# Optimization experiments

Measured on AMD Instinct MI355X. Metric: run time of the kernel, lower is better.

The kernel has to match this reference:

```python
import jax, jax.numpy as jnp
import numpy as np

NUM_HEADS = 12
LN_EPS = 1e-5
SM_EPS = 1e-6


def layer_norm(x, w, b):
    m = x.mean(-1, keepdims=True)
    v = ((x - m) ** 2).mean(-1, keepdims=True)
    return (x - m) / jnp.sqrt(v + LN_EPS) * w + b


def softmax_with_policy(attn, policy):
    # attn: [B,H,N,N], policy: [B,N,1]
    B, H, N, _ = attn.shape
    attn_policy = policy.reshape(B, 1, 1, N)
    eye = jnp.eye(N, dtype=attn.dtype)[None, None]
    attn_policy = attn_policy + (1.0 - attn_policy) * eye
    m = attn.max(axis=-1, keepdims=True)
    e = jnp.exp(attn - m) * attn_policy
    return (e + SM_EPS / N) / (e.sum(axis=-1, keepdims=True) + SM_EPS)


def create_ys(ncdf, n_ref):
    # ncdf: [B, N-1]; returns ys: [B, n_ref-1]
    B = ncdf.shape[0]
    ys = jnp.linspace(0.0, 1.0, n_ref - 1, dtype=ncdf.dtype)[None, :]
    ys_start = jnp.min(ncdf + (ncdf == 0).astype(ncdf.dtype) * 1e8, axis=1, keepdims=True)
    steps = jnp.arange(n_ref - 1, dtype=ncdf.dtype)[None, :]
    return ys_start + (ys * (n_ref - 2) - ys_start * steps) / (n_ref - 2)


def get_unique_indices(indices, max_value):
    # duplicate indices are replaced by max_value, then re-sorted
    B = indices.shape[0]
    s = jnp.sort(indices, axis=1)
    shifted = jnp.concatenate([s[:, 1:], jnp.ones((B, 1), s.dtype)], axis=1)
    uniq = jnp.where(shifted == s, max_value, s)
    return jnp.sort(uniq, axis=1)


def ats_block(x, policy, norm1_w, norm1_b, qkv_w, proj_w, proj_b,
              norm2_w, norm2_b, fc1_w, fc1_b, fc2_w, fc2_b,
              n_tokens, n_ref_tokens):
    B, N, C = x.shape
    H = NUM_HEADS
    dh = C // H
    scale = dh ** -0.5

    xn = layer_norm(x, norm1_w, norm1_b)
    qkv = (xn @ qkv_w).reshape(B, N, 3, H, dh).transpose(2, 0, 3, 1, 4)  # [3,B,H,N,dh]
    qkv = qkv * policy[None, :, None, :, :]
    q, k, v = qkv[0], qkv[1], qkv[2]

    attn = softmax_with_policy(jnp.einsum('bhnd,bhmd->bhnm', q, k) * scale, policy)

    # --- score assignment ---
    v_norm = jnp.linalg.norm(v.transpose(0, 2, 1, 3).reshape(B, N, C), axis=2)  # [B,N]
    sig = attn[:, :, 0, :].sum(axis=1) * v_norm      # CLS attention row summed over heads
    sig = sig[:, 1:]
    sig = sig / sig.sum(axis=1, keepdims=True)
    order = jnp.argsort(sig, axis=1)                 # ascending
    sorted_scores = jnp.take_along_axis(sig, order, axis=1)

    # --- inverse transform sampling ---
    cdf = jnp.cumsum(sorted_scores, axis=1)
    cmin = cdf.min(axis=1, keepdims=True)
    cmax = cdf.max(axis=1, keepdims=True)
    ncdf = (cdf - cmin) / (cmax - cmin)              # [B, N-1]
    ys = create_ys(ncdf, n_ref_tokens)               # [B, n_ref-1]
    diff = (n_ref_tokens - 1) - (N - 1)
    ncdf_p = jnp.pad(ncdf, ((0, 0), (diff, 0))) if diff > 0 else ncdf
    tokens_to_pick = jnp.argmin(jnp.abs(ys[:, :, None] - ncdf_p[:, None, :]), axis=2) - diff

    uniq = get_unique_indices(tokens_to_pick, N - 1)[:, :N - 1]
    ui = uniq[:, :n_tokens - 1]                      # [B, n_tokens-1]

    # reorder attn rows / raw tokens by significance order, pad a zero row at N-1
    oidx = jnp.broadcast_to(order[:, None, :, None], (B, H, N - 1, N))
    attn_sorted = jnp.take_along_axis(attn[:, :, 1:, :], oidx, axis=2)
    attn_tmp = jnp.pad(attn_sorted, ((0, 0), (0, 0), (0, 1), (0, 0)))
    rx_sorted = jnp.take_along_axis(x[:, 1:, :], jnp.broadcast_to(order[:, :, None], (B, N - 1, C)), axis=1)
    rx_tmp = jnp.pad(rx_sorted, ((0, 0), (0, 1), (0, 0)))

    uidx = jnp.broadcast_to(ui[:, None, :, None], (B, H, n_tokens - 1, N))
    attn_sel = jnp.take_along_axis(attn_tmp, uidx, axis=2)
    rx_sel = jnp.take_along_axis(rx_tmp, jnp.broadcast_to(ui[:, :, None], (B, n_tokens - 1, C)), axis=1)

    attn_new = jnp.concatenate([attn[:, :, 0:1, :], attn_sel], axis=2)     # [B,H,n_tokens,N]
    selected_x = jnp.concatenate([x[:, 0:1, :], rx_sel], axis=1)           # [B,n_tokens,C]
    pol_new = (ui != N - 1).astype(x.dtype)[:, :, None]
    pol_new = jnp.pad(pol_new, ((0, 0), (1, 0), (0, 0)), constant_values=1.0)  # [B,n_tokens,1]

    out = jnp.einsum('bhnm,bhmd->bhnd', attn_new, v)
    out = out.transpose(0, 2, 1, 3).reshape(B, n_tokens, C)
    out = (out @ proj_w + proj_b) * pol_new

    x2 = selected_x + out
    h = jax.nn.gelu(layer_norm(x2, norm2_w, norm2_b) @ fc1_w + fc1_b, approximate=False)
    x2 = x2 + (h @ fc2_w + fc2_b) * pol_new
    return x2, pol_new


def setup_inputs() -> dict:
    key = jax.random.key(0)
    ks = jax.random.split(key, 6)
    B, N, C = 8, 785, 768
    init = lambda k, sh, fan: jax.random.normal(k, sh, jnp.float32) * (fan ** -0.5)
    return {
        'x': jax.random.normal(ks[0], (B, N, C), jnp.float32),
        'policy': jnp.ones((B, N, 1), jnp.float32),
        'norm1_w': jnp.ones((C,), jnp.float32),
        'norm1_b': jnp.zeros((C,), jnp.float32),
        'qkv_w': init(ks[1], (C, 3 * C), C),
        'proj_w': init(ks[2], (C, C), C),
        'proj_b': jnp.zeros((C,), jnp.float32),
        'norm2_w': jnp.ones((C,), jnp.float32),
        'norm2_b': jnp.zeros((C,), jnp.float32),
        'fc1_w': init(ks[3], (C, 4 * C), C),
        'fc1_b': jnp.zeros((4 * C,), jnp.float32),
        'fc2_w': init(ks[4], (4 * C, C), 4 * C),
        'fc2_b': jnp.zeros((C,), jnp.float32),
        'n_tokens': 393,
        'n_ref_tokens': 785,
    }


def reference(x, policy, norm1_w, norm1_b, qkv_w, proj_w, proj_b,
              norm2_w, norm2_b, fc1_w, fc1_b, fc2_w, fc2_b,
              n_tokens, n_ref_tokens):
    return ats_block(x, policy, norm1_w, norm1_b, qkv_w, proj_w, proj_b,
                     norm2_w, norm2_b, fc1_w, fc1_b, fc2_w, fc2_b,
                     int(n_tokens), int(n_ref_tokens))
```

## Files before the change

kernel.cpp:

```cpp
#include <hip/hip_runtime.h>
#include <hip/hip_bf16.h>
#include <float.h>
#include <math.h>
#include <stdint.h>

constexpr int B_   = 8;
constexpr int N_   = 785;
constexpr int C_   = 768;
constexpr int H_   = 12;
constexpr int DH_  = 64;
constexpr int NT_  = 393;
constexpr int QKVC = 3 * C_;
constexpr int BN   = B_ * N_;
constexpr int BT   = B_ * NT_;
constexpr int MSEL = N_ - 1;
constexpr float  SCALE_F = 0.125f;
constexpr double LNEPS   = 1e-5;
constexpr double SMEPS   = 1e-6;

#define DEV static __device__ __forceinline__

typedef __hip_bfloat16 bf16;
typedef __attribute__((ext_vector_type(8))) short frag8;
typedef __attribute__((ext_vector_type(4))) float facc4;

DEV double blockReduceSumD(double v, double* scratch, int nw) {
#pragma unroll
  for (int o = 32; o; o >>= 1) v += __shfl_xor(v, o);
  int lane = threadIdx.x & 63, wid = threadIdx.x >> 6;
  __syncthreads();
  if (lane == 0) scratch[wid] = v;
  __syncthreads();
  double r = scratch[0];
  for (int i = 1; i < nw; i++) r += scratch[i];
  return r;
}
DEV double blockReduceMaxD(double v, double* scratch, int nw) {
#pragma unroll
  for (int o = 32; o; o >>= 1) v = fmax(v, __shfl_xor(v, o));
  int lane = threadIdx.x & 63, wid = threadIdx.x >> 6;
  __syncthreads();
  if (lane == 0) scratch[wid] = v;
  __syncthreads();
  double r = scratch[0];
  for (int i = 1; i < nw; i++) r = fmax(r, scratch[i]);
  return r;
}
DEV float blockReduceSumF(float v, float* scratch, int nw) {
#pragma unroll
  for (int o = 32; o; o >>= 1) v += __shfl_xor(v, o);
  int lane = threadIdx.x & 63, wid = threadIdx.x >> 6;
  __syncthreads();
  if (lane == 0) scratch[wid] = v;
  __syncthreads();
  float r = scratch[0];
  for (int i = 1; i < nw; i++) r += scratch[i];
  return r;
}
DEV float blockReduceMaxF(float v, float* scratch, int nw) {
#pragma unroll
  for (int o = 32; o; o >>= 1) v = fmaxf(v, __shfl_xor(v, o));
  int lane = threadIdx.x & 63, wid = threadIdx.x >> 6;
  __syncthreads();
  if (lane == 0) scratch[wid] = v;
  __syncthreads();
  float r = scratch[0];
  for (int i = 1; i < nw; i++) r = fmaxf(r, scratch[i]);
  return r;
}

__global__ __launch_bounds__(256) void ln1_kernel(
    const float* __restrict__ x, const float* __restrict__ w, const float* __restrict__ b,
    double* __restrict__ xn64, bf16* __restrict__ xnb) {
  int row = blockIdx.x;
  int t = threadIdx.x;
  __shared__ double scr[8];
  const float* xr = x + (size_t)row * C_;
  double vals[3];
#pragma unroll
  for (int i = 0; i < 3; i++) vals[i] = (double)xr[t + i * 256];
  double s = vals[0] + vals[1] + vals[2];
  s = blockReduceSumD(s, scr, 4);
  double mean = s / (double)C_;
  double vs = 0.0;
#pragma unroll
  for (int i = 0; i < 3; i++) { double d = vals[i] - mean; vs += d * d; }
  vs = blockReduceSumD(vs, scr, 4);
  double inv = 1.0 / sqrt(vs / (double)C_ + LNEPS);
#pragma unroll
  for (int i = 0; i < 3; i++) {
    int c = t + i * 256;
    double o = (vals[i] - mean) * inv * (double)w[c] + (double)b[c];
    xn64[(size_t)row * C_ + c] = o;
    xnb[(size_t)row * C_ + c] = __float2bfloat16((float)o);
  }
}

__global__ __launch_bounds__(256) void transpose_bf16(
    const float* __restrict__ W, bf16* __restrict__ Wt, int K, int N) {
  __shared__ float tile[32][33];
  int k0 = blockIdx.y * 32, n0 = blockIdx.x * 32;
  int tx = threadIdx.x & 31, ty = threadIdx.x >> 5;
  for (int i = ty; i < 32; i += 8) {
    int k = k0 + i, n = n0 + tx;
    tile[i][tx] = (k < K && n < N) ? W[(size_t)k * N + n] : 0.f;
  }
  __syncthreads();
  for (int i = ty; i < 32; i += 8) {
    int n = n0 + i, k = k0 + tx;
    if (n < N && k < K) Wt[(size_t)n * K + k] = __float2bfloat16(tile[tx][i]);
  }
}

__global__ __launch_bounds__(256) void gemm_bf16(
    const bf16* __restrict__ A, const bf16* __restrict__ Bt,
    float* __restrict__ Cc, const float* __restrict__ bias,
    const float* __restrict__ rowscale, int M, int K, int Ncols) {
  __shared__ short As[64][40];
  __shared__ short Bs[64][40];
  const short* Ap = (const short*)A;
  const short* Bp = (const short*)Bt;
  int t = threadIdx.x;
  int n0 = blockIdx.x * 64;
  int m0 = blockIdx.y * 64;
  int w = t >> 6, l = t & 63;
  int srow = t >> 2;
  int koff = (t & 3) * 8;
  facc4 acc[4] = {{0, 0, 0, 0}, {0, 0, 0, 0}, {0, 0, 0, 0}, {0, 0, 0, 0}};
  int frow = (l & 15);
  int fk = (l >> 4) * 8;
  for (int k0 = 0; k0 < K; k0 += 32) {
    {
      int4 av = make_int4(0, 0, 0, 0);
      if (m0 + srow < M)
        av = *(const int4*)(Ap + (size_t)(m0 + srow) * K + k0 + koff);
      *(int4*)(&As[srow][koff]) = av;
      int4 bv = *(const int4*)(Bp + (size_t)(n0 + srow) * K + k0 + koff);
      *(int4*)(&Bs[srow][koff]) = bv;
    }
    __syncthreads();
    frag8 a = *(frag8*)(&As[w * 16 + frow][fk]);
#pragma unroll
    for (int nt = 0; nt < 4; nt++) {
      frag8 bfr = *(frag8*)(&Bs[nt * 16 + frow][fk]);
      acc[nt] = __builtin_amdgcn_mfma_f32_16x16x32_bf16(a, bfr, acc[nt], 0, 0, 0);
    }
    __syncthreads();
  }
#pragma unroll
  for (int nt = 0; nt < 4; nt++) {
#pragma unroll
    for (int reg = 0; reg < 4; reg++) {
      int row = m0 + w * 16 + (l >> 4) * 4 + reg;
      int col = n0 + nt * 16 + (l & 15);
      if (row < M) {
        float v = acc[nt][reg];
        if (bias) v += bias[col];
        if (rowscale) v *= rowscale[row];
        Cc[(size_t)row * Ncols + col] = v;
      }
    }
  }
}

__global__ __launch_bounds__(256) void q0_kernel(
    const double* __restrict__ xn64, const float* __restrict__ qkvw,
    const float* __restrict__ policy, double* __restrict__ q064) {
  int b = blockIdx.x;
  int jc = blockIdx.y;
  int t = threadIdx.x;
  int jl = t & 63, ks = t >> 6;
  __shared__ double x0[C_];
  __shared__ double part[4][64];
  for (int i = t; i < C_; i += 256) x0[i] = xn64[(size_t)(b * N_) * C_ + i];
  __syncthreads();
  int j = jc * 64 + jl;
  const float* wp = qkvw + j;
  double a = 0.0;
  int c0 = ks * 192;
#pragma unroll 8
  for (int c = c0; c < c0 + 192; c++) a += x0[c] * (double)wp[(size_t)c * QKVC];
  part[ks][jl] = a;
  __syncthreads();
  if (t < 64) {
    double pol = (double)policy[b * N_];
    q064[b * C_ + jc * 64 + t] =
        (part[0][t] + part[1][t] + part[2][t] + part[3][t]) * pol;
  }
}

__global__ __launch_bounds__(256) void g_kernel(
    const double* __restrict__ q064, const float* __restrict__ qkvw,
    double* __restrict__ g64) {
  int bh = blockIdx.x;
  int b = bh / H_, h = bh % H_;
  int t = threadIdx.x;
  __shared__ double qh[DH_];
  if (t < DH_) qh[t] = q064[b * C_ + h * DH_ + t];
  __syncthreads();
  for (int c = t; c < C_; c += 256) {
    const float* wp = qkvw + (size_t)c * QKVC + C_ + h * DH_;
    double a = 0.0;
#pragma unroll 8
    for (int d = 0; d < DH_; d++) a += qh[d] * (double)wp[d];
    g64[(size_t)bh * C_ + c] = a;
  }
}

__global__ __launch_bounds__(256) void logits_kernel(
    const double* __restrict__ xn64, const double* __restrict__ g64,
    const float* __restrict__ policy, double* __restrict__ l64) {
  int row = blockIdx.x;
  int b = row / N_;
  int n = row % N_;
  int t = threadIdx.x;
  int w = t >> 6, lane = t & 63;
  __shared__ double xr[C_];
  for (int i = t; i < C_; i += 256) xr[i] = xn64[(size_t)row * C_ + i];
  __syncthreads();
  double pol = (double)policy[row];
#pragma unroll
  for (int hh = 0; hh < 3; hh++) {
    int h = w + hh * 4;
    const double* gp = g64 + (size_t)(b * H_ + h) * C_;
    double p = 0.0;
#pragma unroll 4
    for (int i = lane; i < C_; i += 64) p += xr[i] * gp[i];
#pragma unroll
    for (int o = 32; o; o >>= 1) p += __shfl_xor(p, o);
    if (lane == 0) l64[(size_t)(b * H_ + h) * N_ + n] = 0.125 * pol * p;
  }
}

__global__ __launch_bounds__(256) void vnorm_kernel(
    const double* __restrict__ xn64, const float* __restrict__ qkvw,
    double* __restrict__ vnp3) {
  __shared__ double scr[8];
  int r0 = blockIdx.x * 8;
  int chunk = blockIdx.y;
  int t = threadIdx.x;
  double acc[8] = {};
  const double* xb = xn64 + (size_t)r0 * C_;
  const float* wcol = qkvw + 2 * C_ + chunk * 256 + t;
  for (int c = 0; c < C_; c += 2) {
    double w0 = (double)wcol[(size_t)c * QKVC];
    double w1 = (double)wcol[(size_t)(c + 1) * QKVC];
#pragma unroll
    for (int r = 0; r < 8; r++) {
      double x0 = xb[(size_t)r * C_ + c];
      double x1 = xb[(size_t)r * C_ + c + 1];
      acc[r] += x0 * w0;
      acc[r] += x1 * w1;
    }
  }
#pragma unroll
  for (int r = 0; r < 8; r++) {
    double p = acc[r] * acc[r];
    double s = blockReduceSumD(p, scr, 4);
    if (t == 0) vnp3[(size_t)chunk * BN + r0 + r] = s;
  }
}

__global__ __launch_bounds__(256) void vnorm_combine_kernel(
    const double* __restrict__ vnp3, const float* __restrict__ policy,
    double* __restrict__ vnorm2) {
  int row = blockIdx.x * 256 + threadIdx.x;
  if (row >= BN) return;
  double s = vnp3[row] + vnp3[(size_t)BN + row] + vnp3[(size_t)2 * BN + row];
  double pol = (double)policy[row];
  vnorm2[row] = s * pol * pol;
}

__global__ __launch_bounds__(256) void softmax0_kernel(
    double* __restrict__ l64, const float* __restrict__ policy) {
  int bh = blockIdx.x;
  int b = bh / H_;
  double* lp = l64 + (size_t)bh * N_;
  __shared__ double scr[8];
  int t = threadIdx.x;
  double mx = -1e300;
  for (int n = t; n < N_; n += 256) mx = fmax(mx, lp[n]);
  mx = blockReduceMaxD(mx, scr, 4);
  double ssum = 0.0;
  for (int n = t; n < N_; n += 256) {
    double pol = (double)policy[b * N_ + n];
    double w = (n == 0) ? 1.0 : pol;
    double e = exp(lp[n] - mx) * w;
    lp[n] = e;
    ssum += e;
  }
  ssum = blockReduceSumD(ssum, scr, 4);
  double denom = ssum + SMEPS;
  double addc = SMEPS / (double)N_;
  for (int n = t; n < N_; n += 256) lp[n] = (lp[n] + addc) / denom;
}

__global__ __launch_bounds__(1024) void select_kernel(
    const double* __restrict__ p0, const double* __restrict__ vnorm2,
    int* __restrict__ selidx, float* __restrict__ poln, float* __restrict__ out_pol) {
  int b = blockIdx.x;
  int t = threadIdx.x;
  __shared__ double sigv[MSEL];
  __shared__ double svals[MSEL];
  __shared__ double nc[MSEL];
  __shared__ int    ord[MSEL];
  __shared__ int    pick[MSEL];
  __shared__ int    spick[MSEL];
  __shared__ int    uq[MSEL];
  __shared__ int    suq[MSEL];
  __shared__ double sh_ys;

  if (t < MSEL) {
    int n = t + 1;
    double s = 0.0;
#pragma unroll
    for (int h = 0; h < H_; h++) s += p0[(size_t)(b * H_ + h) * N_ + n];
    sigv[t] = s * sqrt(vnorm2[b * N_ + n]);
  }
  __syncthreads();
  if (t < MSEL) {
    double v = sigv[t];
    int rank = 0;
    for (int i = 0; i < MSEL; i++) {
      double vi = sigv[i];
      rank += (vi < v) || (vi == v && i < t);
    }
    ord[rank] = t;
    svals[rank] = v;
  }
  __syncthreads();
  if (t == 0) {
    double a = 0.0;
    for (int i = 0; i < MSEL; i++) { a += svals[i]; svals[i] = a; }
  }
  __syncthreads();
  {
    double c0 = svals[0], cN = svals[MSEL - 1];
    if (t < MSEL) nc[t] = (svals[t] - c0) / (cN - c0);
  }
  __syncthreads();
  if (t == 0) {
    double m = 1e300;
    for (int i = 0; i < MSEL; i++) {
      double v = nc[i];
      if (v == 0.0) v += 100000000.0;
      m = fmin(m, v);
    }
    sh_ys = m;
  }
  __syncthreads();
  if (t < MSEL) {
    double s = sh_ys;
    double ysj = (t == MSEL - 1) ? 1.0 : (double)t / 783.0;
    double y = s + (ysj * 783.0 - s * (double)t) / 783.0;
    double bd = 1e300;
    int bi = 0;
    for (int i = 0; i < MSEL; i++) {
      double d = fabs(y - nc[i]);
      if (d < bd) { bd = d; bi = i; }
    }
    pick[t] = bi;
  }
  __syncthreads();
  if (t < MSEL) {
    int p = pick[t];
    int rank = 0;
    for (int i = 0; i < MSEL; i++) {
      int pi = pick[i];
      rank += (pi < p) || (pi == p && i < t);
    }
    spick[rank] = p;
  }
  __syncthreads();
  if (t < MSEL) {
    int s = spick[t];
    int nxt = (t < MSEL - 1) ? spick[t + 1] : 1;
    uq[t] = (nxt == s) ? MSEL : s;
  }
  __syncthreads();
  if (t < MSEL) {
    int u = uq[t];
    int rank = 0;
    for (int i = 0; i < MSEL; i++) {
      int ui = uq[i];
      rank += (ui < u) || (ui == u && i < t);
    }
    suq[rank] = u;
  }
  __syncthreads();
  if (t < NT_) {
    int sel, polI;
    if (t == 0) { sel = 0; polI = 1; }
    else {
      int ut = suq[t - 1];
      polI = (ut != MSEL) ? 1 : 0;
      sel = polI ? (ord[ut] + 1) : -1;
    }
    selidx[b * NT_ + t] = sel;
    poln[b * NT_ + t] = (float)polI;
    out_pol[b * NT_ + t] = (float)polI;
  }
}

__global__ __launch_bounds__(256) void flash_kernel(
    const float* __restrict__ qkv, const int* __restrict__ selidx,
    const float* __restrict__ policy, bf16* __restrict__ attn_bf) {
  int bh = blockIdx.y;
  int b = bh / H_, h = bh % H_;
  int j0 = blockIdx.x * 64;
  int t = threadIdx.x;
  __shared__ float Qs[64][68];
  __shared__ float KVs[64][68];
  __shared__ float Ps[64][68];
  __shared__ float Vsum[64];
  int lm = t >> 2;
  int kb = (t & 3) * 16;
  {
    int j = j0 + lm;
    int r = (j < NT_) ? selidx[b * NT_ + j] : -1;
    if (r < 0) r = 0;
    const float* qp = qkv + (size_t)(b * N_ + r) * QKVC + h * DH_ + kb;
    float4 v0 = *(const float4*)(qp + 0);
    float4 v1 = *(const float4*)(qp + 4);
    float4 v2 = *(const float4*)(qp + 8);
    float4 v3 = *(const float4*)(qp + 12);
    Qs[kb + 0][lm] = v0.x; Qs[kb + 1][lm] = v0.y; Qs[kb + 2][lm] = v0.z; Qs[kb + 3][lm] = v0.w;
    Qs[kb + 4][lm] = v1.x; Qs[kb + 5][lm] = v1.y; Qs[kb + 6][lm] = v1.z; Qs[kb + 7][lm] = v1.w;
    Qs[kb + 8][lm] = v2.x; Qs[kb + 9][lm] = v2.y; Qs[kb +10][lm] = v2.z; Qs[kb +11][lm] = v2.w;
    Qs[kb +12][lm] = v3.x; Qs[kb +13][lm] = v3.y; Qs[kb +14][lm] = v3.z; Qs[kb +15][lm] = v3.w;
  }
  if (t < 64) Vsum[t] = 0.f;
  int tm = (t >> 4) << 2, tn = (t & 15) << 2;
  int rrow[4];
#pragma unroll
  for (int i = 0; i < 4; i++) {
    int j = j0 + tm + i;
    rrow[i] = (j < NT_) ? selidx[b * NT_ + j] : -1;
  }
  float m_run[4] = {-1e30f, -1e30f, -1e30f, -1e30f};
  float s_run[4] = {0.f, 0.f, 0.f, 0.f};
  float O[4][4] = {{0.f}};
  for (int n0 = 0; n0 < 832; n0 += 64) {
    __syncthreads();
    {
      int n = n0 + lm;
      bool ok = n < N_;
      const float* kp = qkv + (size_t)(b * N_ + (ok ? n : 0)) * QKVC + C_ + h * DH_ + kb;
      float4 v0 = ok ? *(const float4*)(kp + 0)  : make_float4(0, 0, 0, 0);
      float4 v1 = ok ? *(const float4*)(kp + 4)  : make_float4(0, 0, 0, 0);
      float4 v2 = ok ? *(const float4*)(kp + 8)  : make_float4(0, 0, 0, 0);
      float4 v3 = ok ? *(const float4*)(kp + 12) : make_float4(0, 0, 0, 0);
      KVs[kb + 0][lm] = v0.x; KVs[kb + 1][lm] = v0.y; KVs[kb + 2][lm] = v0.z; KVs[kb + 3][lm] = v0.w;
      KVs[kb + 4][lm] = v1.x; KVs[kb + 5][lm] = v1.y; KVs[kb + 6][lm] = v1.z; KVs[kb + 7][lm] = v1.w;
      KVs[kb + 8][lm] = v2.x; KVs[kb + 9][lm] = v2.y; KVs[kb +10][lm] = v2.z; KVs[kb +11][lm] = v2.w;
      KVs[kb +12][lm] = v3.x; KVs[kb +13][lm] = v3.y; KVs[kb +14][lm] = v3.z; KVs[kb +15][lm] = v3.w;
    }
    __syncthreads();
    float S[4][4] = {{0.f}};
#pragma unroll 16
    for (int k = 0; k < 64; k++) {
      float a0 = Qs[k][tm + 0], a1 = Qs[k][tm + 1], a2 = Qs[k][tm + 2], a3 = Qs[k][tm + 3];
      float b0 = KVs[k][tn + 0], b1 = KVs[k][tn + 1], b2 = KVs[k][tn + 2], b3 = KVs[k][tn + 3];
      S[0][0] += a0 * b0; S[0][1] += a0 * b1; S[0][2] += a0 * b2; S[0][3] += a0 * b3;
      S[1][0] += a1 * b0; S[1][1] += a1 * b1; S[1][2] += a1 * b2; S[1][3] += a1 * b3;
      S[2][0] += a2 * b0; S[2][1] += a2 * b1; S[2][2] += a2 * b2; S[2][3] += a2 * b3;
      S[3][0] += a3 * b0; S[3][1] += a3 * b1; S[3][2] += a3 * b2; S[3][3] += a3 * b3;
    }
    float tmax[4];
#pragma unroll
    for (int i = 0; i < 4; i++) {
      float mx = -1e30f;
#pragma unroll
      for (int jj = 0; jj < 4; jj++) {
        int n = n0 + tn + jj;
        float v = (n < N_) ? S[i][jj] * SCALE_F : -1e30f;
        S[i][jj] = v;
        mx = fmaxf(mx, v);
      }
      tmax[i] = mx;
    }
#pragma unroll
    for (int o = 1; o < 16; o <<= 1) {
#pragma unroll
      for (int i = 0; i < 4; i++) tmax[i] = fmaxf(tmax[i], __shfl_xor(tmax[i], o));
    }
    float m_new[4], scl[4], psum[4];
#pragma unroll
    for (int i = 0; i < 4; i++) {
      m_new[i] = fmaxf(m_run[i], tmax[i]);
      scl[i] = expf(m_run[i] - m_new[i]);
      psum[i] = 0.f;
    }
    float polv[4];
#pragma unroll
    for (int jj = 0; jj < 4; jj++) {
      int n = n0 + tn + jj;
      polv[jj] = (n < N_) ? policy[b * N_ + n] : 0.f;
    }
#pragma unroll
    for (int i = 0; i < 4; i++) {
#pragma unroll
      for (int jj = 0; jj < 4; jj++) {
        int n = n0 + tn + jj;
        float w = (n == rrow[i]) ? 1.f : polv[jj];
        float e = expf(S[i][jj] - m_new[i]) * w;
        S[i][jj] = e;
        psum[i] += e;
      }
    }
#pragma unroll
    for (int o = 1; o < 16; o <<= 1) {
#pragma unroll
      for (int i = 0; i < 4; i++) psum[i] += __shfl_xor(psum[i], o);
    }
#pragma unroll
    for (int i = 0; i < 4; i++) {
      s_run[i] = s_run[i] * scl[i] + psum[i];
      m_run[i] = m_new[i];
    }
    __syncthreads();
#pragma unroll
    for (int i = 0; i < 4; i++) {
#pragma unroll
      for (int jj = 0; jj < 4; jj++) Ps[tn + jj][tm + i] = S[i][jj];
    }
    {
      int n = n0 + lm;
      bool ok = n < N_;
      const float* vp = qkv + (size_t)(b * N_ + (ok ? n : 0)) * QKVC + 2 * C_ + h * DH_ + kb;
      float4 v0 = ok ? *(const float4*)(vp + 0)  : make_float4(0, 0, 0, 0);
      float4 v1 = ok ? *(const float4*)(vp + 4)  : make_float4(0, 0, 0, 0);
      float4 v2 = ok ? *(const float4*)(vp + 8)  : make_float4(0, 0, 0, 0);
      float4 v3 = ok ? *(const float4*)(vp + 12) : make_float4(0, 0, 0, 0);
      *(float4*)(&KVs[lm][kb + 0])  = v0;
      *(float4*)(&KVs[lm][kb + 4])  = v1;
      *(float4*)(&KVs[lm][kb + 8])  = v2;
      *(float4*)(&KVs[lm][kb + 12]) = v3;
    }
    __syncthreads();
    if (t < 64) {
      float a = 0.f;
#pragma unroll 16
      for (int k = 0; k < 64; k++) a += KVs[k][t];
      Vsum[t] += a;
    }
#pragma unroll
    for (int i = 0; i < 4; i++) {
#pragma unroll
      for (int jj = 0; jj < 4; jj++) O[i][jj] *= scl[i];
    }
#pragma unroll 16
    for (int k = 0; k < 64; k++) {
      float a0 = Ps[k][tm + 0], a1 = Ps[k][tm + 1], a2 = Ps[k][tm + 2], a3 = Ps[k][tm + 3];
      float b0 = KVs[k][tn + 0], b1 = KVs[k][tn + 1], b2 = KVs[k][tn + 2], b3 = KVs[k][tn + 3];
      O[0][0] += a0 * b0; O[0][1] += a0 * b1; O[0][2] += a0 * b2; O[0][3] += a0 * b3;
      O[1][0] += a1 * b0; O[1][1] += a1 * b1; O[1][2] += a1 * b2; O[1][3] += a1 * b3;
      O[2][0] += a2 * b0; O[2][1] += a2 * b1; O[2][2] += a2 * b2; O[2][3] += a2 * b3;
      O[3][0] += a3 * b0; O[3][1] += a3 * b1; O[3][2] += a3 * b2; O[3][3] += a3 * b3;
    }
  }
  __syncthreads();
  float addc = 1e-6f / (float)N_;
#pragma unroll
  for (int i = 0; i < 4; i++) {
    int j = j0 + tm + i;
    if (j >= NT_) continue;
    float denom = s_run[i] + 1e-6f;
#pragma unroll
    for (int jj = 0; jj < 4; jj++) {
      float val = (O[i][jj] + addc * Vsum[tn + jj]) / denom;
      attn_bf[(size_t)(b * NT_ + j) * C_ + h * DH_ + tn + jj] = __float2bfloat16(val);
    }
  }
}

__global__ __launch_bounds__(256) void e2_kernel(
    const float* __restrict__ cbuf, const float* __restrict__ poln,
    const int* __restrict__ selidx, const float* __restrict__ x, float* __restrict__ x2) {
  int row = blockIdx.x;
  int t = threadIdx.x;
  int b = row / NT_;
  int r = selidx[row];
  float pn = poln[row];
  for (int i = t; i < C_; i += 256) {
    float sx = (r >= 0) ? x[(size_t)(b * N_ + r) * C_ + i] : 0.f;
    x2[(size_t)row * C_ + i] = sx + cbuf[(size_t)row * C_ + i] * pn;
  }
}

__global__ __launch_bounds__(256) void ln2_kernel(
    const float* __restrict__ xin, const float* __restrict__ w, const float* __restrict__ b,
    bf16* __restrict__ xoutb) {
  int row = blockIdx.x;
  int t = threadIdx.x;
  __shared__ float scr[8];
  const float* xr = xin + (size_t)row * C_;
  float vals[3];
#pragma unroll
  for (int i = 0; i < 3; i++) vals[i] = xr[t + i * 256];
  float s = vals[0] + vals[1] + vals[2];
  s = blockReduceSumF(s, scr, 4);
  float mean = s / (float)C_;
  float vs = 0.f;
#pragma unroll
  for (int i = 0; i < 3; i++) { float d = vals[i] - mean; vs += d * d; }
  vs = blockReduceSumF(vs, scr, 4);
  float sd = sqrtf(vs / (float)C_ + 1e-5f);
#pragma unroll
  for (int i = 0; i < 3; i++) {
    int c = t + i * 256;
    xoutb[(size_t)row * C_ + c] =
        __float2bfloat16((vals[i] - mean) / sd * w[c] + b[c]);
  }
}

DEV float gelu_exact(float v) { return 0.5f * v * (1.0f + erff(v * 0.70710678118654752f)); }

__global__ __launch_bounds__(256) void gelu_kernel(
    const float* __restrict__ h, bf16* __restrict__ hb) {
  size_t i = (size_t)blockIdx.x * 256 + threadIdx.x;
  float4 v = ((const float4*)h)[i];
  ushort4 o;
  o.x = __hip_bfloat16_raw(__float2bfloat16(gelu_exact(v.x))).x;
  o.y = __hip_bfloat16_raw(__float2bfloat16(gelu_exact(v.y))).x;
  o.z = __hip_bfloat16_raw(__float2bfloat16(gelu_exact(v.z))).x;
  o.w = __hip_bfloat16_raw(__float2bfloat16(gelu_exact(v.w))).x;
  ((ushort4*)hb)[i] = o;
}

__global__ __launch_bounds__(256) void e4_kernel(
    const float* __restrict__ x2, const float* __restrict__ cbuf,
    const float* __restrict__ poln, float* __restrict__ out) {
  int row = blockIdx.x;
  int t = threadIdx.x;
  float pn = poln[row];
  for (int i = t; i < C_; i += 256) {
    float v = x2[(size_t)row * C_ + i] + cbuf[(size_t)row * C_ + i] * pn;
    out[(size_t)row * C_ + i] = v;
  }
}

extern "C" void kernel_launch(void* const* d_in, const int* in_sizes, int n_in,
                              void* d_out, int out_size, void* d_ws, size_t ws_size,
                              hipStream_t stream) {
  const float* x      = (const float*)d_in[0];
  const float* policy = (const float*)d_in[1];
  const float* n1w    = (const float*)d_in[2];
  const float* n1b    = (const float*)d_in[3];
  const float* qkvw   = (const float*)d_in[4];
  const float* projw  = (const float*)d_in[5];
  const float* projb  = (const float*)d_in[6];
  const float* n2w    = (const float*)d_in[7];
  const float* n2b    = (const float*)d_in[8];
  const float* fc1w   = (const float*)d_in[9];
  const float* fc1b   = (const float*)d_in[10];
  const float* fc2w   = (const float*)d_in[11];
  const float* fc2b   = (const float*)d_in[12];

  char* ws = (char*)d_ws;
  size_t off = 0;
  auto alloc = [&](size_t bytes) {
    size_t o = off;
    off += (bytes + 255) & ~(size_t)255;
    return o;
  };

  double* xn64    = (double*)(ws + alloc((size_t)BN * C_ * 8));
  bf16*   xnb     = (bf16*)(ws + alloc((size_t)BN * C_ * 2));
  float*  qkv32   = (float*)(ws + alloc((size_t)BN * QKVC * 4));
  double* vnorm2  = (double*)(ws + alloc((size_t)BN * 8));
  double* vnp3    = (double*)(ws + alloc((size_t)3 * BN * 8));
  double* q064    = (double*)(ws + alloc((size_t)B_ * C_ * 8));
  double* g64     = (double*)(ws + alloc((size_t)B_ * H_ * C_ * 8));
  double* l64     = (double*)(ws + alloc((size_t)B_ * H_ * N_ * 8));
  int*    selidx  = (int*)(ws + alloc((size_t)BT * 4));
  float*  poln    = (float*)(ws + alloc((size_t)BT * 4));
  bf16*   attn_bf = (bf16*)(ws + alloc((size_t)BT * C_ * 2));
  float*  cbuf    = (float*)(ws + alloc((size_t)BT * C_ * 4));
  float*  x2      = (float*)(ws + alloc((size_t)BT * C_ * 4));
  bf16*   qkvw_t  = (bf16*)(ws + alloc((size_t)QKVC * C_ * 2));
  bf16*   projw_t = (bf16*)(ws + alloc((size_t)C_ * C_ * 2));
  bf16*   fc1w_t  = (bf16*)(ws + alloc((size_t)4 * C_ * C_ * 2));
  bf16*   fc2w_t  = (bf16*)(ws + alloc((size_t)C_ * 4 * C_ * 2));
  bf16*   xn2b    = (bf16*)(ws + alloc((size_t)BT * C_ * 2));
  float*  h32     = (float*)(ws + alloc((size_t)BT * 4 * C_ * 4));
  bf16*   h_bf    = (bf16*)(ws + alloc((size_t)BT * 4 * C_ * 2));
  if (off > ws_size) return;

  float* out_x = (float*)d_out;
  float* out_p = out_x + (size_t)BT * C_;

  transpose_bf16<<<dim3(QKVC / 32, C_ / 32), 256, 0, stream>>>(qkvw, qkvw_t, C_, QKVC);
  transpose_bf16<<<dim3(C_ / 32, C_ / 32), 256, 0, stream>>>(projw, projw_t, C_, C_);
  transpose_bf16<<<dim3(4 * C_ / 32, C_ / 32), 256, 0, stream>>>(fc1w, fc1w_t, C_, 4 * C_);
  transpose_bf16<<<dim3(C_ / 32, 4 * C_ / 32), 256, 0, stream>>>(fc2w, fc2w_t, 4 * C_, C_);

  ln1_kernel<<<BN, 256, 0, stream>>>(x, n1w, n1b, xn64, xnb);

  {
    dim3 g(QKVC / 64, (BN + 63) / 64);
    gemm_bf16<<<g, 256, 0, stream>>>(xnb, qkvw_t, qkv32, nullptr, policy, BN, C_, QKVC);
  }

  q0_kernel<<<dim3(B_, C_ / 64), 256, 0, stream>>>(xn64, qkvw, policy, q064);
  g_kernel<<<B_ * H_, 256, 0, stream>>>(q064, qkvw, g64);
  logits_kernel<<<BN, 256, 0, stream>>>(xn64, g64, policy, l64);
  vnorm_kernel<<<dim3(BN / 8, 3), 256, 0, stream>>>(xn64, qkvw, vnp3);
  vnorm_combine_kernel<<<(BN + 255) / 256, 256, 0, stream>>>(vnp3, policy, vnorm2);
  softmax0_kernel<<<B_ * H_, 256, 0, stream>>>(l64, policy);
  select_kernel<<<B_, 1024, 0, stream>>>(l64, vnorm2, selidx, poln, out_p);

  {
    dim3 g((NT_ + 63) / 64, B_ * H_);
    flash_kernel<<<g, 256, 0, stream>>>(qkv32, selidx, policy, attn_bf);
  }

  {
    dim3 g(C_ / 64, (BT + 63) / 64);
    gemm_bf16<<<g, 256, 0, stream>>>(attn_bf, projw_t, cbuf, projb, nullptr, BT, C_, C_);
  }
  e2_kernel<<<BT, 256, 0, stream>>>(cbuf, poln, selidx, x, x2);
  ln2_kernel<<<BT, 256, 0, stream>>>(x2, n2w, n2b, xn2b);
  {
    dim3 g(4 * C_ / 64, (BT + 63) / 64);
    gemm_bf16<<<g, 256, 0, stream>>>(xn2b, fc1w_t, h32, fc1b, nullptr, BT, C_, 4 * C_);
  }
  gelu_kernel<<<(BT * 4 * C_) / 1024, 256, 0, stream>>>(h32, h_bf);
  {
    dim3 g(C_ / 64, (BT + 63) / 64);
    gemm_bf16<<<g, 256, 0, stream>>>(h_bf, fc2w_t, cbuf, fc2b, nullptr, BT, 4 * C_, C_);
  }
  e4_kernel<<<BT, 256, 0, stream>>>(x2, cbuf, poln, out_x);
}
```

Baseline: 996.6 us.

## Restructure fp64 V-norm GEMM with transposed activations and per-lane row tiling

Rewrites the double-precision V-norm computation so that xn64 is first transposed into a padded column-major buffer and the V slice of qkv_w is pre-converted to fp64. Each lane now owns one row and accumulates 16 output columns, with weights broadcast uniformly across the wavefront and coalesced x loads. This replaces the old scheme, where every block streamed strided fp32 weight columns and reduced across the whole block for each of 8 rows. In exchange it adds a transpose kernel, a conversion kernel, extra workspace, and a 12-way partial-sum combine.

```diff
diff --git a/kernel.cpp b/kernel.cpp
--- a/kernel.cpp
+++ b/kernel.cpp
@@ -12,6 +12,7 @@
 constexpr int NT_  = 393;
 constexpr int QKVC = 3 * C_;
 constexpr int BN   = B_ * N_;
+constexpr int BNP  = 6336;
 constexpr int BT   = B_ * NT_;
 constexpr int MSEL = N_ - 1;
 constexpr float  SCALE_F = 0.125f;
@@ -110,6 +111,27 @@
     int n = n0 + i, k = k0 + tx;
     if (n < N && k < K) Wt[(size_t)n * K + k] = __float2bfloat16(tile[tx][i]);
   }
+}
+
+__global__ __launch_bounds__(256) void xpose64_kernel(
+    const double* __restrict__ xn64, double* __restrict__ xn64T) {
+  __shared__ double tile[32][33];
+  int r0 = blockIdx.x * 32, c0 = blockIdx.y * 32;
+  int tx = threadIdx.x & 31, ty = threadIdx.x >> 5;
+  for (int i = ty; i < 32; i += 8) {
+    int r = r0 + i;
+    tile[i][tx] = (r < BN) ? xn64[(size_t)r * C_ + c0 + tx] : 0.0;
+  }
+  __syncthreads();
+  for (int i = ty; i < 32; i += 8)
+    xn64T[(size_t)(c0 + i) * BNP + r0 + tx] = tile[tx][i];
+}
+
+__global__ __launch_bounds__(256) void wvcvt_kernel(
+    const float* __restrict__ qkvw, double* __restrict__ wv64) {
+  int idx = blockIdx.x * 256 + threadIdx.x;
+  int c = idx / 768, j = idx - c * 768;
+  wv64[idx] = (double)qkvw[(size_t)c * QKVC + 2 * C_ + j];
 }
 
 __global__ __launch_bounds__(256) void gemm_bf16(
@@ -233,40 +255,44 @@
 }
 
 __global__ __launch_bounds__(256) void vnorm_kernel(
-    const double* __restrict__ xn64, const float* __restrict__ qkvw,
-    double* __restrict__ vnp3) {
-  __shared__ double scr[8];
-  int r0 = blockIdx.x * 8;
-  int chunk = blockIdx.y;
-  int t = threadIdx.x;
-  double acc[8] = {};
-  const double* xb = xn64 + (size_t)r0 * C_;
-  const float* wcol = qkvw + 2 * C_ + chunk * 256 + t;
-  for (int c = 0; c < C_; c += 2) {
-    double w0 = (double)wcol[(size_t)c * QKVC];
-    double w1 = (double)wcol[(size_t)(c + 1) * QKVC];
-#pragma unroll
-    for (int r = 0; r < 8; r++) {
-      double x0 = xb[(size_t)r * C_ + c];
-      double x1 = xb[(size_t)r * C_ + c + 1];
-      acc[r] += x0 * w0;
-      acc[r] += x1 * w1;
-    }
-  }
-#pragma unroll
-  for (int r = 0; r < 8; r++) {
-    double p = acc[r] * acc[r];
-    double s = blockReduceSumD(p, scr, 4);
-    if (t == 0) vnp3[(size_t)chunk * BN + r0 + r] = s;
+    const double* __restrict__ xn64T, const double* __restrict__ wv64,
+    double* __restrict__ vnp) {
+  __shared__ double part[4][64];
+  int r0 = blockIdx.x * 64;
+  int jt = blockIdx.y;
+  int t = threadIdx.x;
+  int lane = t & 63;
+  int w = __builtin_amdgcn_readfirstlane(t >> 6);
+  const double* xcol = xn64T + r0 + lane;
+  const double* wrow = wv64 + jt * 64 + w * 16;
+  double acc[16] = {};
+  for (int c = 0; c < C_; c++) {
+    double xv = xcol[(size_t)c * BNP];
+    const double* wp = wrow + (size_t)c * C_;
+#pragma unroll
+    for (int j = 0; j < 16; j++) acc[j] += xv * wp[j];
+  }
+  double p = 0.0;
+#pragma unroll
+  for (int j = 0; j < 16; j++) p += acc[j] * acc[j];
+  part[w][lane] = p;
+  __syncthreads();
+  if (t < 64) {
+    int row = r0 + t;
+    if (row < BN)
+      vnp[(size_t)jt * BNP + row] =
+          part[0][t] + part[1][t] + part[2][t] + part[3][t];
   }
 }
 
 __global__ __launch_bounds__(256) void vnorm_combine_kernel(
-    const double* __restrict__ vnp3, const float* __restrict__ policy,
+    const double* __restrict__ vnp, const float* __restrict__ policy,
     double* __restrict__ vnorm2) {
   int row = blockIdx.x * 256 + threadIdx.x;
   if (row >= BN) return;
-  double s = vnp3[row] + vnp3[(size_t)BN + row] + vnp3[(size_t)2 * BN + row];
+  double s = 0.0;
+#pragma unroll
+  for (int jt = 0; jt < 12; jt++) s += vnp[(size_t)jt * BNP + row];
   double pol = (double)policy[row];
   vnorm2[row] = s * pol * pol;
 }
@@ -666,10 +692,12 @@
   };
 
   double* xn64    = (double*)(ws + alloc((size_t)BN * C_ * 8));
+  double* xn64T   = (double*)(ws + alloc((size_t)C_ * BNP * 8));
+  double* wv64    = (double*)(ws + alloc((size_t)C_ * C_ * 8));
   bf16*   xnb     = (bf16*)(ws + alloc((size_t)BN * C_ * 2));
   float*  qkv32   = (float*)(ws + alloc((size_t)BN * QKVC * 4));
   double* vnorm2  = (double*)(ws + alloc((size_t)BN * 8));
-  double* vnp3    = (double*)(ws + alloc((size_t)3 * BN * 8));
+  double* vnp     = (double*)(ws + alloc((size_t)12 * BNP * 8));
   double* q064    = (double*)(ws + alloc((size_t)B_ * C_ * 8));
   double* g64     = (double*)(ws + alloc((size_t)B_ * H_ * C_ * 8));
   double* l64     = (double*)(ws + alloc((size_t)B_ * H_ * N_ * 8));
@@ -694,8 +722,10 @@
   transpose_bf16<<<dim3(C_ / 32, C_ / 32), 256, 0, stream>>>(projw, projw_t, C_, C_);
   transpose_bf16<<<dim3(4 * C_ / 32, C_ / 32), 256, 0, stream>>>(fc1w, fc1w_t, C_, 4 * C_);
   transpose_bf16<<<dim3(C_ / 32, 4 * C_ / 32), 256, 0, stream>>>(fc2w, fc2w_t, 4 * C_, C_);
+  wvcvt_kernel<<<(C_ * C_) / 256, 256, 0, stream>>>(qkvw, wv64);
 
   ln1_kernel<<<BN, 256, 0, stream>>>(x, n1w, n1b, xn64, xnb);
+  xpose64_kernel<<<dim3(BNP / 32, C_ / 32), 256, 0, stream>>>(xn64, xn64T);
 
   {
     dim3 g(QKVC / 64, (BN + 63) / 64);
@@ -705,8 +735,8 @@
   q0_kernel<<<dim3(B_, C_ / 64), 256, 0, stream>>>(xn64, qkvw, policy, q064);
   g_kernel<<<B_ * H_, 256, 0, stream>>>(q064, qkvw, g64);
   logits_kernel<<<BN, 256, 0, stream>>>(xn64, g64, policy, l64);
-  vnorm_kernel<<<dim3(BN / 8, 3), 256, 0, stream>>>(xn64, qkvw, vnp3);
-  vnorm_combine_kernel<<<(BN + 255) / 256, 256, 0, stream>>>(vnp3, policy, vnorm2);
+  vnorm_kernel<<<dim3(BNP / 64, 12), 256, 0, stream>>>(xn64T, wv64, vnp);
+  vnorm_combine_kernel<<<(BN + 255) / 256, 256, 0, stream>>>(vnp, policy, vnorm2);
   softmax0_kernel<<<B_ * H_, 256, 0, stream>>>(l64, policy);
   select_kernel<<<B_, 1024, 0, stream>>>(l64, vnorm2, selidx, poln, out_p);
 
```

After: 995.1 us. No clear change (-0.2%).
